# Optimization experiments

Measured on AMD Instinct MI355X. Metric: run time of the kernel, lower is better.

## Reference

```python
import jax, jax.numpy as jnp
import numpy as np

N_EMB = 1024
N_HEAD = 16
HEAD_DIM = N_EMB // N_HEAD


def setup_inputs() -> dict:
    key = jax.random.key(0)
    ks = jax.random.split(key, 5)
    scale = 0.02
    x = jax.random.normal(ks[0], (2, 2048, N_EMB), dtype=jnp.float32)
    W_attn = jax.random.normal(ks[1], (N_EMB, 3 * N_EMB), dtype=jnp.float32) * scale
    b_attn = jnp.zeros((3 * N_EMB,), dtype=jnp.float32)
    W_proj = jax.random.normal(ks[2], (N_EMB, N_EMB), dtype=jnp.float32) * scale
    b_proj = jnp.zeros((N_EMB,), dtype=jnp.float32)
    return {"x": x, "W_attn": W_attn, "b_attn": b_attn, "W_proj": W_proj, "b_proj": b_proj}


def reference(x, W_attn, b_attn, W_proj, b_proj):
    B, T, C = x.shape
    qkv = x @ W_attn + b_attn  # [B, T, 3C]
    q, k, v = jnp.split(qkv, 3, axis=-1)
    # [B, H, T, Dh]
    q = q.reshape(B, T, N_HEAD, HEAD_DIM).transpose(0, 2, 1, 3)
    k = k.reshape(B, T, N_HEAD, HEAD_DIM).transpose(0, 2, 1, 3)
    v = v.reshape(B, T, N_HEAD, HEAD_DIM).transpose(0, 2, 1, 3)
    scale = 1.0 / jnp.sqrt(jnp.float32(HEAD_DIM))
    attn = jnp.einsum('bhqd,bhkd->bhqk', q, k) * scale  # [B, H, T, T]
    causal = jnp.tril(jnp.ones((T, T), dtype=bool))
    attn = jnp.where(causal[None, None], attn, -jnp.inf)
    attn = jax.nn.softmax(attn, axis=-1)
    y = jnp.einsum('bhqk,bhkd->bhqd', attn, v)  # [B, H, T, Dh]
    y = y.transpose(0, 2, 1, 3).reshape(B, T, C)
    return y @ W_proj + b_proj
```

## Files before the change

kernel.cpp:

```cpp
#include <hip/hip_runtime.h>
#include <hip/hip_bf16.h>

typedef __bf16 bf16;
typedef __attribute__((ext_vector_type(2))) __bf16 bf16x2;
typedef __attribute__((ext_vector_type(4))) __bf16 bf16x4;
typedef __attribute__((ext_vector_type(8))) __bf16 bf16x8;
typedef __attribute__((ext_vector_type(4))) float f32x4;
typedef __attribute__((ext_vector_type(16))) float f32x16;
typedef unsigned int u32;
typedef __attribute__((ext_vector_type(4))) u32 u32x4;
typedef const __attribute__((address_space(1))) u32* gptr_t;
typedef __attribute__((address_space(3))) u32* lptr_t;

#define N_EMB 1024
#define N_HEAD 16
#define HEAD_DIM 64
#define T_SEQ 2048
#define BATCH 2
#define M_TOT (BATCH * T_SEQ)
#define N_QKV (3 * N_EMB)
#define KDIM 1024
#define CS_LOG2E 0.1803368801111129f

__device__ inline unsigned short f2bu(float f) {
    unsigned u = __builtin_bit_cast(unsigned, f);
    return (unsigned short)((u + 0x7fffu + ((u >> 16) & 1u)) >> 16);
}
__device__ inline bf16 f2b(float f) {
    unsigned short s = f2bu(f);
    return __builtin_bit_cast(bf16, s);
}
__device__ inline u32 pkbf(float lo, float hi) {
    bf16x2 t; t[0] = (bf16)lo; t[1] = (bf16)hi;
    return __builtin_bit_cast(u32, t);
}
__device__ __forceinline__ float xhalf_sum(float x) {
    return x + __shfl_xor(x, 32, 64);
}

__global__ __launch_bounds__(256) void k_cast(const float* __restrict__ x,
                                              bf16* __restrict__ xb, int n4) {
    int i = blockIdx.x * 256 + threadIdx.x;
    if (i < n4) {
        float4 v = reinterpret_cast<const float4*>(x)[i];
        ushort4 u;
        u.x = f2bu(v.x); u.y = f2bu(v.y); u.z = f2bu(v.z); u.w = f2bu(v.w);
        reinterpret_cast<ushort4*>(xb)[i] = u;
    }
}

__global__ __launch_bounds__(256) void k_transpose(const float* __restrict__ W,
                                                   bf16* __restrict__ Wt,
                                                   int K, int N) {
    __shared__ float tile[32][33];
    int k0 = blockIdx.x * 32;
    int n0 = blockIdx.y * 32;
    int tx = threadIdx.x & 31;
    int ty = threadIdx.x >> 5;
    for (int j = 0; j < 32; j += 8)
        tile[ty + j][tx] = W[(k0 + ty + j) * N + n0 + tx];
    __syncthreads();
    for (int j = 0; j < 32; j += 8)
        Wt[(n0 + ty + j) * (long)K + k0 + tx] = f2b(tile[tx][ty + j]);
}

__global__ __launch_bounds__(256) void k_vtrans(const bf16* __restrict__ v,
                                                bf16* __restrict__ vt) {
    __shared__ bf16 tile[64 * 76];
    const int bh = blockIdx.y;
    const int t0 = blockIdx.x * 64;
    const bf16* src = v + (size_t)bh * T_SEQ * HEAD_DIM;
    bf16* dst = vt + (size_t)bh * HEAD_DIM * T_SEQ;
    const int tid = threadIdx.x;
    #pragma unroll
    for (int it = 0; it < 2; ++it) {
        const int row = (tid >> 3) + it * 32;
        const int col = (tid & 7) * 8;
        bf16x8 val = *reinterpret_cast<const bf16x8*>(src + (size_t)(t0 + row) * HEAD_DIM + col);
        bf16x4 lo;  lo[0] = val[0]; lo[1] = val[1]; lo[2] = val[2]; lo[3] = val[3];
        bf16x4 hiv; hiv[0] = val[4]; hiv[1] = val[5]; hiv[2] = val[6]; hiv[3] = val[7];
        *reinterpret_cast<bf16x4*>(&tile[row * 76 + col]) = lo;
        *reinterpret_cast<bf16x4*>(&tile[row * 76 + col + 4]) = hiv;
    }
    __syncthreads();
    #pragma unroll
    for (int it = 0; it < 2; ++it) {
        const int d  = (tid >> 3) + it * 32;
        const int tt = (tid & 7) * 8;
        bf16x8 val;
        #pragma unroll
        for (int q = 0; q < 8; ++q) {
            const int pq = tt + q;
            const int sw = ((pq >> 2) ^ (pq >> 3)) & 1;
            const int ps = sw ? (pq ^ 12) : pq;
            val[q] = tile[ps * 76 + d];
        }
        *reinterpret_cast<bf16x8*>(dst + (size_t)d * T_SEQ + t0 + tt) = val;
    }
}

#define GEMM_MAINLOOP(A_, Bt_, m0_, n0_)                                          \
    __shared__ __align__(16) bf16 As[128 * 32];                                   \
    __shared__ __align__(16) bf16 Bs[128 * 32];                                   \
    const int lane = threadIdx.x & 63;                                            \
    const int w    = threadIdx.x >> 6;                                            \
    const int wr   = w >> 1;                                                      \
    const int wc   = w & 1;                                                       \
    const int r    = lane & 15;                                                   \
    const int ko   = (lane >> 4) * 8;                                             \
    const int srow = w * 32 + (lane >> 2);                                        \
    const int sk   = (lane & 3) * 8;                                              \
    const bf16* a_g0 = A_ + (size_t)(m0_ + srow) * KDIM + sk;                     \
    const bf16* a_g1 = a_g0 + 16 * KDIM;                                          \
    const bf16* b_g0 = Bt_ + (size_t)(n0_ + srow) * KDIM + sk;                    \
    const bf16* b_g1 = b_g0 + 16 * KDIM;                                          \
    bf16* a_l0 = As + (w * 2) * 512;                                              \
    bf16* a_l1 = As + (w * 2 + 1) * 512;                                          \
    bf16* b_l0 = Bs + (w * 2) * 512;                                              \
    bf16* b_l1 = Bs + (w * 2 + 1) * 512;                                          \
    f32x4 acc[4][4];                                                              \
    for (int i = 0; i < 4; ++i)                                                   \
        for (int j = 0; j < 4; ++j) acc[i][j] = (f32x4){0.f, 0.f, 0.f, 0.f};      \
    for (int k0 = 0; k0 < KDIM; k0 += 32) {                                       \
        __builtin_amdgcn_global_load_lds((gptr_t)(const void*)(a_g0 + k0),        \
                                         (lptr_t)(void*)a_l0, 16, 0, 0);          \
        __builtin_amdgcn_global_load_lds((gptr_t)(const void*)(a_g1 + k0),        \
                                         (lptr_t)(void*)a_l1, 16, 0, 0);          \
        __builtin_amdgcn_global_load_lds((gptr_t)(const void*)(b_g0 + k0),        \
                                         (lptr_t)(void*)b_l0, 16, 0, 0);          \
        __builtin_amdgcn_global_load_lds((gptr_t)(const void*)(b_g1 + k0),        \
                                         (lptr_t)(void*)b_l1, 16, 0, 0);          \
        __syncthreads();                                                          \
        bf16x8 af[4], bfr[4];                                                     \
        for (int m = 0; m < 4; ++m)                                               \
            af[m] = *reinterpret_cast<const bf16x8*>(As + (wr * 64 + m * 16 + r) * 32 + ko); \
        for (int n = 0; n < 4; ++n)                                               \
            bfr[n] = *reinterpret_cast<const bf16x8*>(Bs + (wc * 64 + n * 16 + r) * 32 + ko); \
        for (int m = 0; m < 4; ++m)                                               \
            for (int n = 0; n < 4; ++n)                                           \
                acc[m][n] = __builtin_amdgcn_mfma_f32_16x16x32_bf16(af[m], bfr[n], acc[m][n], 0, 0, 0); \
        __syncthreads();                                                          \
    }

#define GEMM_MAINLOOP_64(A_, Bt_, m0_, n0_)                                       \
    __shared__ __align__(16) bf16 As[64 * 32];                                    \
    __shared__ __align__(16) bf16 Bs[128 * 32];                                   \
    const int lane = threadIdx.x & 63;                                            \
    const int w    = threadIdx.x >> 6;                                            \
    const int wr   = w >> 1;                                                      \
    const int wc   = w & 1;                                                       \
    const int r    = lane & 15;                                                   \
    const int ko   = (lane >> 4) * 8;                                             \
    const int srow = w * 16 + (lane >> 2);                                        \
    const int sk   = (lane & 3) * 8;                                              \
    const bf16* a_g0 = A_ + (size_t)(m0_ + srow) * KDIM + sk;                     \
    const bf16* b_g0 = Bt_ + (size_t)(n0_ + srow) * KDIM + sk;                    \
    const bf16* b_g1 = b_g0 + 64 * KDIM;                                          \
    bf16* a_l0 = As + w * 512;                                                    \
    bf16* b_l0 = Bs + w * 512;                                                    \
    bf16* b_l1 = Bs + 64 * 32 + w * 512;                                          \
    f32x4 acc[2][4];                                                              \
    for (int i = 0; i < 2; ++i)                                                   \
        for (int j = 0; j < 4; ++j) acc[i][j] = (f32x4){0.f, 0.f, 0.f, 0.f};      \
    for (int k0 = 0; k0 < KDIM; k0 += 32) {                                       \
        __builtin_amdgcn_global_load_lds((gptr_t)(const void*)(a_g0 + k0),        \
                                         (lptr_t)(void*)a_l0, 16, 0, 0);          \
        __builtin_amdgcn_global_load_lds((gptr_t)(const void*)(b_g0 + k0),        \
                                         (lptr_t)(void*)b_l0, 16, 0, 0);          \
        __builtin_amdgcn_global_load_lds((gptr_t)(const void*)(b_g1 + k0),        \
                                         (lptr_t)(void*)b_l1, 16, 0, 0);          \
        __syncthreads();                                                          \
        bf16x8 af[2], bfr[4];                                                     \
        for (int m = 0; m < 2; ++m)                                               \
            af[m] = *reinterpret_cast<const bf16x8*>(As + (wr * 32 + m * 16 + r) * 32 + ko); \
        for (int n = 0; n < 4; ++n)                                               \
            bfr[n] = *reinterpret_cast<const bf16x8*>(Bs + (wc * 64 + n * 16 + r) * 32 + ko); \
        for (int m = 0; m < 2; ++m)                                               \
            for (int n = 0; n < 4; ++n)                                           \
                acc[m][n] = __builtin_amdgcn_mfma_f32_16x16x32_bf16(af[m], bfr[n], acc[m][n], 0, 0, 0); \
        __syncthreads();                                                          \
    }

__global__ __launch_bounds__(256) void k_gemm_qkv(const bf16* __restrict__ A,
                                                  const bf16* __restrict__ Bt,
                                                  const float* __restrict__ bias,
                                                  bf16* __restrict__ qb,
                                                  bf16* __restrict__ kb,
                                                  bf16* __restrict__ vb) {
    const int m0 = blockIdx.x * 128;
    const int n0 = blockIdx.y * 128;
    GEMM_MAINLOOP(A, Bt, m0, n0)
    const int col   = lane & 15;
    const int rbase = (lane >> 4) * 4;
    for (int nn = 0; nn < 4; ++nn) {
        int n = n0 + wc * 64 + nn * 16 + col;
        float bv = bias[n];
        int which = n >> 10;
        int c  = n & 1023;
        int h  = c >> 6;
        int dh = c & 63;
        bf16* dst = (which == 0) ? qb : ((which == 1) ? kb : vb);
        const float sc = (which == 0) ? CS_LOG2E : 1.0f;
        for (int mm = 0; mm < 4; ++mm) {
            for (int i = 0; i < 4; ++i) {
                int m = m0 + wr * 64 + mm * 16 + rbase + i;
                int b_ = m >> 11;
                int t  = m & 2047;
                dst[(((b_ * N_HEAD + h) * T_SEQ) + t) * HEAD_DIM + dh] =
                    f2b((acc[mm][nn][i] + bv) * sc);
            }
        }
    }
}

__global__ __launch_bounds__(256) void k_gemm_proj(const bf16* __restrict__ A,
                                                   const bf16* __restrict__ Bt,
                                                   const float* __restrict__ bias,
                                                   float* __restrict__ out) {
    const int m0 = blockIdx.x * 64;
    const int n0 = blockIdx.y * 128;
    GEMM_MAINLOOP_64(A, Bt, m0, n0)
    const int col   = lane & 15;
    const int rbase = (lane >> 4) * 4;
    for (int nn = 0; nn < 4; ++nn) {
        int n = n0 + wc * 64 + nn * 16 + col;
        float bv = bias[n];
        for (int mm = 0; mm < 2; ++mm) {
            for (int i = 0; i < 4; ++i) {
                int m = m0 + wr * 32 + mm * 16 + rbase + i;
                out[(size_t)m * N_EMB + n] = acc[mm][nn][i] + bv;
            }
        }
    }
}

__device__ __forceinline__ void pv_group(const float* p,
                                         const bf16x8 (&va)[2][2], f32x16 (&o)[2]) {
    u32x4 f0, f1;
    f0[0] = pkbf(p[0], p[1]);   f0[1] = pkbf(p[2], p[3]);
    f0[2] = pkbf(p[4], p[5]);   f0[3] = pkbf(p[6], p[7]);
    f1[0] = pkbf(p[8], p[9]);   f1[1] = pkbf(p[10], p[11]);
    f1[2] = pkbf(p[12], p[13]); f1[3] = pkbf(p[14], p[15]);
    bf16x8 pb0 = __builtin_bit_cast(bf16x8, f0);
    bf16x8 pb1 = __builtin_bit_cast(bf16x8, f1);
    __builtin_amdgcn_s_setprio(1);
    #pragma unroll
    for (int dt = 0; dt < 2; ++dt) {
        o[dt] = __builtin_amdgcn_mfma_f32_32x32x16_bf16(va[dt][0], pb0, o[dt], 0, 0, 0);
        o[dt] = __builtin_amdgcn_mfma_f32_32x32x16_bf16(va[dt][1], pb1, o[dt], 0, 0, 0);
    }
    __builtin_amdgcn_s_setprio(0);
}

__device__ __forceinline__ void tile32_lds(const char* Ks, const char* Vs, int g,
                                           int qr, int hi, const bf16x8 (&qf)[4],
                                           bool diag, float& l_r, f32x16 (&o)[2]) {
    const int swz = (qr & 7) << 4;
    bf16x8 kf[4];
    #pragma unroll
    for (int f = 0; f < 4; ++f)
        kf[f] = *reinterpret_cast<const bf16x8*>(
            Ks + (((g * 32 + qr) * 128 + f * 32 + hi * 16) ^ swz));
    f32x16 st;
    #pragma unroll
    for (int r = 0; r < 16; ++r) st[r] = 0.f;
    __builtin_amdgcn_s_setprio(1);
    #pragma unroll
    for (int f = 0; f < 4; ++f)
        st = __builtin_amdgcn_mfma_f32_32x32x16_bf16(kf[f], qf[f], st, 0, 0, 0);
    __builtin_amdgcn_s_setprio(0);
    if (diag) {
        const int kp4 = 4 * hi;
        #pragma unroll
        for (int r = 0; r < 16; ++r) {
            const int kpos = (r & 3) + 8 * (r >> 2) + kp4;
            if (kpos > qr) st[r] = -3.0e38f;
        }
    }
    bf16x8 va[2][2];
    #pragma unroll
    for (int dt = 0; dt < 2; ++dt)
        #pragma unroll
        for (int ks = 0; ks < 2; ++ks)
            va[dt][ks] = *reinterpret_cast<const bf16x8*>(
                Vs + (((dt * 32 + qr) * 128 + g * 64 + ks * 32 + hi * 16) ^ swz));
    float p[16];
    #pragma unroll
    for (int r = 0; r < 16; ++r) p[r] = exp2f(fminf(st[r], 24.f));
    float s = 0.f;
    #pragma unroll
    for (int r = 0; r < 8; ++r) s += p[r] + p[r + 8];
    l_r += s;
    pv_group(p, va, o);
}

__global__ __launch_bounds__(256) void k_attn(const bf16* __restrict__ qb,
                                              const bf16* __restrict__ kb,
                                              const bf16* __restrict__ vtb,
                                              bf16* __restrict__ yb) {
    const int lane = threadIdx.x & 63;
    const int wv   = threadIdx.x >> 6;
    const int bh   = blockIdx.x;
    const int qg   = 15 - blockIdx.y;
    const int qblk = qg * 4 + wv;
    const int q0   = qblk * 32;
    const int b    = bh >> 4;
    const int h    = bh & 15;

    const bf16* Q  = qb  + (size_t)bh * T_SEQ * HEAD_DIM;
    const char* Kg = (const char*)(kb  + (size_t)bh * T_SEQ * HEAD_DIM);
    const char* Vg = (const char*)(vtb + (size_t)bh * HEAD_DIM * T_SEQ);

    const int qr = lane & 31;
    const int hi = lane >> 5;

    bf16x8 qf[4];
    #pragma unroll
    for (int f = 0; f < 4; ++f)
        qf[f] = *reinterpret_cast<const bf16x8*>(
            Q + (size_t)(q0 + qr) * HEAD_DIM + f * 16 + hi * 8);

    f32x16 o[2];
    #pragma unroll
    for (int r = 0; r < 16; ++r) { o[0][r] = 0.f; o[1][r] = 0.f; }
    float l_r = 0.f;

    __shared__ __align__(16) char Ks[8192];
    __shared__ __align__(16) char Vs[8192];

    const int myn    = qblk + 1;
    const int maxT64 = 2 * qg + 2;

    for (int t64 = 0; t64 < maxT64; ++t64) {
        #pragma unroll
        for (int rr = 0; rr < 2; ++rr) {
            const int base = rr * 4096 + wv * 1024;
            const int fb   = base + lane * 16;
            const int row  = fb >> 7;
            const int swz  = (row & 7) << 4;
            __builtin_amdgcn_global_load_lds(
                (gptr_t)(const void*)(Kg + (size_t)t64 * 8192 + (fb ^ swz)),
                (lptr_t)(void*)(Ks + base), 16, 0, 0);
            __builtin_amdgcn_global_load_lds(
                (gptr_t)(const void*)(Vg + (size_t)row * (T_SEQ * 2) + t64 * 128
                                      + ((fb & 127) ^ swz)),
                (lptr_t)(void*)(Vs + base), 16, 0, 0);
        }
        __syncthreads();
        const int kb0 = t64 * 2;
        const int kb1 = kb0 + 1;
        if (kb0 < myn) tile32_lds(Ks, Vs, 0, qr, hi, qf, kb0 == qblk, l_r, o);
        if (kb1 < myn) tile32_lds(Ks, Vs, 1, qr, hi, qf, kb1 == qblk, l_r, o);
        __syncthreads();
    }

    l_r = xhalf_sum(l_r);
    const float inv = 1.f / fmaxf(l_r, 1e-30f);
    const int tq = q0 + qr;
    bf16* yrow = yb + ((size_t)(b * T_SEQ + tq)) * N_EMB + h * HEAD_DIM;
    #pragma unroll
    for (int dt = 0; dt < 2; ++dt) {
        #pragma unroll
        for (int rr = 0; rr < 4; ++rr) {
            const int d0 = dt * 32 + 8 * rr + 4 * hi;
            ushort4 u;
            u.x = f2bu(o[dt][4 * rr + 0] * inv);
            u.y = f2bu(o[dt][4 * rr + 1] * inv);
            u.z = f2bu(o[dt][4 * rr + 2] * inv);
            u.w = f2bu(o[dt][4 * rr + 3] * inv);
            *reinterpret_cast<ushort4*>(yrow + d0) = u;
        }
    }
}

extern "C" void kernel_launch(void* const* d_in, const int* in_sizes, int n_in,
                              void* d_out, int out_size, void* d_ws, size_t ws_size,
                              hipStream_t stream) {
    const float* x      = (const float*)d_in[0];
    const float* W_attn = (const float*)d_in[1];
    const float* b_attn = (const float*)d_in[2];
    const float* W_proj = (const float*)d_in[3];
    const float* b_proj = (const float*)d_in[4];
    float* out = (float*)d_out;

    const size_t sz_x   = (size_t)M_TOT * N_EMB;
    const size_t sz_wat = (size_t)N_QKV * N_EMB;
    const size_t sz_wpt = (size_t)N_EMB * N_EMB;
    const size_t sz_hd  = (size_t)BATCH * N_HEAD * T_SEQ * HEAD_DIM;
    const size_t need = (sz_x + sz_wat + sz_wpt + 3 * sz_hd + sz_x) * sizeof(bf16);
    if (ws_size < need) return;

    bf16* xb  = (bf16*)d_ws;
    bf16* wat = xb + sz_x;
    bf16* wpt = wat + sz_wat;
    bf16* qb  = wpt + sz_wpt;
    bf16* kbf = qb + sz_hd;
    bf16* vbf = kbf + sz_hd;
    bf16* yb  = vbf + sz_hd;
    bf16* vtb = xb;

    k_cast<<<dim3((sz_x / 4 + 255) / 256), 256, 0, stream>>>(x, xb, (int)(sz_x / 4));
    k_transpose<<<dim3(N_EMB / 32, N_QKV / 32), 256, 0, stream>>>(W_attn, wat, N_EMB, N_QKV);
    k_transpose<<<dim3(N_EMB / 32, N_EMB / 32), 256, 0, stream>>>(W_proj, wpt, N_EMB, N_EMB);
    k_gemm_qkv<<<dim3(M_TOT / 128, N_QKV / 128), 256, 0, stream>>>(xb, wat, b_attn, qb, kbf, vbf);
    k_vtrans<<<dim3(T_SEQ / 64, BATCH * N_HEAD), 256, 0, stream>>>(vbf, vtb);
    k_attn<<<dim3(BATCH * N_HEAD, 16), 256, 0, stream>>>(qb, kbf, vtb, yb);
    k_gemm_proj<<<dim3(M_TOT / 64, N_EMB / 128), 256, 0, stream>>>(yb, wpt, b_proj, out);
}
```

Measured before the change: 134.1 us.

## Split attention KV range across waves per query block with LDS reduction

Each workgroup now handles a single 32-row query block, and its four waves split the causal key range between them (split-K). Each wave stages its own K/V tiles into a private LDS slab with no block-wide barriers in the loop. The partial outputs and row sums are then reduced through LDS by wave 0. This is meant to balance causal work across waves and quadruple the grid. In exchange, each wave waits on its own loads with no overlap, three waves go idle during the final reduction, and there is extra LDS traffic. The kernel never uses a running max, so the partial sums can be added directly.

```diff
diff --git a/kernel.cpp b/kernel.cpp
--- a/kernel.cpp
+++ b/kernel.cpp
@@ -252,15 +252,39 @@
     __builtin_amdgcn_s_setprio(0);
 }
 
-__device__ __forceinline__ void tile32_lds(const char* Ks, const char* Vs, int g,
-                                           int qr, int hi, const bf16x8 (&qf)[4],
-                                           bool diag, float& l_r, f32x16 (&o)[2]) {
-    const int swz = (qr & 7) << 4;
+__device__ __forceinline__ void stage_k32(const char* Kg, char* Ks, int kbase, int lane) {
+    #pragma unroll
+    for (int rr = 0; rr < 4; ++rr) {
+        const int fb  = rr * 1024 + lane * 16;
+        const int row = fb >> 7;
+        const int swz = (row & 7) << 4;
+        __builtin_amdgcn_global_load_lds(
+            (gptr_t)(const void*)(Kg + (size_t)kbase * 128 + (fb ^ swz)),
+            (lptr_t)(void*)(Ks + rr * 1024), 16, 0, 0);
+    }
+}
+__device__ __forceinline__ void stage_v32(const char* Vg, char* Vs, int kbase, int lane) {
+    #pragma unroll
+    for (int rr = 0; rr < 4; ++rr) {
+        const int fb  = rr * 1024 + lane * 16;
+        const int d   = fb >> 6;
+        const int off = fb & 63;
+        const int swz = (d & 3) << 4;
+        __builtin_amdgcn_global_load_lds(
+            (gptr_t)(const void*)(Vg + (size_t)d * (T_SEQ * 2) + (size_t)kbase * 2 + (off ^ swz)),
+            (lptr_t)(void*)(Vs + rr * 1024), 16, 0, 0);
+    }
+}
+
+__device__ __forceinline__ void tile32_w(const char* Ks, const char* Vs,
+                                         int qr, int hi, const bf16x8 (&qf)[4],
+                                         bool diag, float& l_r, f32x16 (&o)[2]) {
+    const int swzk = (qr & 7) << 4;
     bf16x8 kf[4];
     #pragma unroll
     for (int f = 0; f < 4; ++f)
         kf[f] = *reinterpret_cast<const bf16x8*>(
-            Ks + (((g * 32 + qr) * 128 + f * 32 + hi * 16) ^ swz));
+            Ks + ((qr * 128 + f * 32 + hi * 16) ^ swzk));
     f32x16 st;
     #pragma unroll
     for (int r = 0; r < 16; ++r) st[r] = 0.f;
@@ -281,9 +305,11 @@
     #pragma unroll
     for (int dt = 0; dt < 2; ++dt)
         #pragma unroll
-        for (int ks = 0; ks < 2; ++ks)
+        for (int ks = 0; ks < 2; ++ks) {
+            const int d = dt * 32 + qr;
             va[dt][ks] = *reinterpret_cast<const bf16x8*>(
-                Vs + (((dt * 32 + qr) * 128 + g * 64 + ks * 32 + hi * 16) ^ swz));
+                Vs + ((d * 64 + ks * 32 + hi * 16) ^ ((d & 3) << 4)));
+        }
     float p[16];
     #pragma unroll
     for (int r = 0; r < 16; ++r) p[r] = exp2f(fminf(st[r], 24.f));
@@ -301,60 +327,76 @@
     const int lane = threadIdx.x & 63;
     const int wv   = threadIdx.x >> 6;
     const int bh   = blockIdx.x;
-    const int qg   = 15 - blockIdx.y;
-    const int qblk = qg * 4 + wv;
+    const int qblk = 63 - blockIdx.y;
     const int q0   = qblk * 32;
     const int b    = bh >> 4;
     const int h    = bh & 15;
 
-    const bf16* Q  = qb  + (size_t)bh * T_SEQ * HEAD_DIM;
+    const char* Qg = (const char*)(qb  + (size_t)bh * T_SEQ * HEAD_DIM);
     const char* Kg = (const char*)(kb  + (size_t)bh * T_SEQ * HEAD_DIM);
     const char* Vg = (const char*)(vtb + (size_t)bh * HEAD_DIM * T_SEQ);
 
     const int qr = lane & 31;
     const int hi = lane >> 5;
 
+    __shared__ __align__(16) char sbuf[4][8192];
+    __shared__ float ls_l[4][64];
+    char* Ks = sbuf[wv];
+    char* Vs = sbuf[wv] + 4096;
+
+    stage_k32(Qg, Ks, qblk * 32, lane);
+    asm volatile("s_waitcnt vmcnt(0)" ::: "memory");
     bf16x8 qf[4];
-    #pragma unroll
-    for (int f = 0; f < 4; ++f)
-        qf[f] = *reinterpret_cast<const bf16x8*>(
-            Q + (size_t)(q0 + qr) * HEAD_DIM + f * 16 + hi * 8);
+    {
+        const int swzk = (qr & 7) << 4;
+        #pragma unroll
+        for (int f = 0; f < 4; ++f)
+            qf[f] = *reinterpret_cast<const bf16x8*>(
+                Ks + ((qr * 128 + f * 32 + hi * 16) ^ swzk));
+    }
 
     f32x16 o[2];
     #pragma unroll
     for (int r = 0; r < 16; ++r) { o[0][r] = 0.f; o[1][r] = 0.f; }
     float l_r = 0.f;
 
-    __shared__ __align__(16) char Ks[8192];
-    __shared__ __align__(16) char Vs[8192];
-
-    const int myn    = qblk + 1;
-    const int maxT64 = 2 * qg + 2;
-
-    for (int t64 = 0; t64 < maxT64; ++t64) {
-        #pragma unroll
-        for (int rr = 0; rr < 2; ++rr) {
-            const int base = rr * 4096 + wv * 1024;
-            const int fb   = base + lane * 16;
-            const int row  = fb >> 7;
-            const int swz  = (row & 7) << 4;
-            __builtin_amdgcn_global_load_lds(
-                (gptr_t)(const void*)(Kg + (size_t)t64 * 8192 + (fb ^ swz)),
-                (lptr_t)(void*)(Ks + base), 16, 0, 0);
-            __builtin_amdgcn_global_load_lds(
-                (gptr_t)(const void*)(Vg + (size_t)row * (T_SEQ * 2) + t64 * 128
-                                      + ((fb & 127) ^ swz)),
-                (lptr_t)(void*)(Vs + base), 16, 0, 0);
-        }
-        __syncthreads();
-        const int kb0 = t64 * 2;
-        const int kb1 = kb0 + 1;
-        if (kb0 < myn) tile32_lds(Ks, Vs, 0, qr, hi, qf, kb0 == qblk, l_r, o);
-        if (kb1 < myn) tile32_lds(Ks, Vs, 1, qr, hi, qf, kb1 == qblk, l_r, o);
-        __syncthreads();
-    }
-
+    const int n    = qblk + 1;
+    const int base = n >> 2;
+    const int rem  = n & 3;
+    const int lo   = wv * base + (wv < rem ? wv : rem);
+    const int cnt  = base + (wv < rem ? 1 : 0);
+    const int end  = lo + cnt;
+
+    for (int t = lo; t < end; ++t) {
+        stage_k32(Kg, Ks, t * 32, lane);
+        stage_v32(Vg, Vs, t * 32, lane);
+        asm volatile("s_waitcnt vmcnt(0)" ::: "memory");
+        tile32_w(Ks, Vs, qr, hi, qf, t == qblk, l_r, o);
+    }
+
+    float* slab = (float*)sbuf[wv];
+    if (wv > 0) {
+        #pragma unroll
+        for (int i = 0; i < 16; ++i) {
+            slab[i * 64 + lane]        = o[0][i];
+            slab[(16 + i) * 64 + lane] = o[1][i];
+        }
+        ls_l[wv][lane] = l_r;
+    }
+    __syncthreads();
+    if (wv > 0) return;
+    #pragma unroll
+    for (int s = 1; s < 4; ++s) {
+        const float* sl = (const float*)sbuf[s];
+        l_r += ls_l[s][lane];
+        #pragma unroll
+        for (int i = 0; i < 16; ++i) {
+            o[0][i] += sl[i * 64 + lane];
+            o[1][i] += sl[(16 + i) * 64 + lane];
+        }
+    }
     l_r = xhalf_sum(l_r);
+
     const float inv = 1.f / fmaxf(l_r, 1e-30f);
     const int tq = q0 + qr;
     bf16* yrow = yb + ((size_t)(b * T_SEQ + tq)) * N_EMB + h * HEAD_DIM;
@@ -404,6 +446,6 @@
     k_transpose<<<dim3(N_EMB / 32, N_EMB / 32), 256, 0, stream>>>(W_proj, wpt, N_EMB, N_EMB);
     k_gemm_qkv<<<dim3(M_TOT / 128, N_QKV / 128), 256, 0, stream>>>(xb, wat, b_attn, qb, kbf, vbf);
     k_vtrans<<<dim3(T_SEQ / 64, BATCH * N_HEAD), 256, 0, stream>>>(vbf, vtb);
-    k_attn<<<dim3(BATCH * N_HEAD, 16), 256, 0, stream>>>(qb, kbf, vtb, yb);
+    k_attn<<<dim3(BATCH * N_HEAD, 64), 256, 0, stream>>>(qb, kbf, vtb, yb);
     k_gemm_proj<<<dim3(M_TOT / 64, N_EMB / 128), 256, 0, stream>>>(yb, wpt, b_proj, out);
 }
```

New measurement: 117.3 us. -12.6%, faster.
